# Optimization experiments

Hardware: AMD Instinct MI355X
Metric: run time of the kernel (lower is better)

The kernel has to match this reference:

```python
import jax, jax.numpy as jnp
import numpy as np

B, D_IN, HID, DEPTH = 16384, 128, 16, 8
N_INNER = 2 ** DEPTH - 1   # 255
N_LEAF = 2 ** DEPTH        # 256


def setup_inputs() -> dict:
    key = jax.random.key(0)
    ks = jax.random.split(key, 4)
    x = jax.random.normal(ks[0], (B, D_IN), jnp.float32)
    # Batched per-inner-node tiny MLP parameters (PyTorch stores one Sequential per node;
    # we stack them along a leading node axis so the math is identical but vectorized).
    W1 = jax.random.normal(ks[1], (N_INNER, D_IN, HID), jnp.float32) / np.sqrt(D_IN).astype(np.float32)
    b1 = jnp.zeros((N_INNER, HID), jnp.float32)
    W2 = jax.random.normal(ks[2], (N_INNER, HID), jnp.float32) / np.sqrt(HID).astype(np.float32)
    b2 = jnp.zeros((N_INNER,), jnp.float32)
    leaf = jax.random.normal(ks[3], (N_LEAF, 1), jnp.float32) * 0.1
    return {"x": x, "W1": W1, "b1": b1, "W2": W2, "b2": b2, "leaf": leaf}


def reference(x, W1, b1, W2, b2, leaf):
    b = x.shape[0]
    depth = int(np.log2(leaf.shape[0]))
    # All inner-node gates in one batched GEMM: p[b, n] = sigmoid(W2_n . relu(W1_n^T x_b + b1_n) + b2_n)
    h1 = jax.nn.relu(jnp.einsum('bi,nih->bnh', x, W1) + b1[None])  # [B, N_inner, hid]
    p = jax.nn.sigmoid(jnp.einsum('bnh,nh->bn', h1, W2) + b2[None])  # [B, N_inner]

    # Level-by-level probability propagation (heap-ordered nodes):
    # children of node j are 2j+1 (left, mass*(1-p)) and 2j+2 (right, mass*p).
    r = jnp.ones((b, 1), x.dtype)
    levels = []
    for l in range(depth):
        levels.append(r)
        pl = p[:, 2 ** l - 1: 2 ** (l + 1) - 1]  # probs of nodes at level l, [B, 2^l]
        # interleave (left, right) so child ordering matches heap indexing
        r = jnp.stack([r * (1.0 - pl), r * pl], axis=-1).reshape(b, 2 ** (l + 1))
    node_reach = jnp.concatenate(levels, axis=1)  # [B, N_inner]
    path_probs = r                                 # [B, N_leaf]

    h = (path_probs @ leaf)[:, 0]                  # [B]
    return (h, path_probs, p, node_reach)
```

## Files before the change

### kernel.cpp

```cpp
#include <hip/hip_runtime.h>

#define BATCH 16384
#define DIN   128
#define HIDN  16
#define NNODE 255
#define NLEAF 256
#define TR    16

typedef _Float16 half8 __attribute__((ext_vector_type(8)));
typedef _Float16 half4 __attribute__((ext_vector_type(4)));
typedef float   float4v __attribute__((ext_vector_type(4)));

__global__ __launch_bounds__(256) void k_pack(const float* __restrict__ x, const float* __restrict__ w1,
                                              const float* __restrict__ w2,
                                              half8* __restrict__ xp, half8* __restrict__ w1p,
                                              _Float16* __restrict__ w2h) {
    __shared__ float w[DIN * 17];
    int t = threadIdx.x;
    if (blockIdx.x < 1024) {
        int gid  = blockIdx.x * 256 + t;
        int lane = gid & 63;
        int kc   = (gid >> 6) & 3;
        int bt   = gid >> 8;
        const float4* src = (const float4*)(x + (size_t)(bt * 16 + (lane & 15)) * DIN + kc * 32 + ((lane >> 4) * 8));
        float4 v0 = src[0], v1 = src[1];
        half8 v;
        v[0] = (_Float16)v0.x; v[1] = (_Float16)v0.y; v[2] = (_Float16)v0.z; v[3] = (_Float16)v0.w;
        v[4] = (_Float16)v1.x; v[5] = (_Float16)v1.y; v[6] = (_Float16)v1.z; v[7] = (_Float16)v1.w;
        xp[gid] = v;
    } else {
        int n = blockIdx.x - 1024;
        const float4* src = (const float4*)(w1 + (size_t)n * (DIN * HIDN)) + t * 2;
        float4 a0 = src[0], a1 = src[1];
        int base = t * 8;
#pragma unroll
        for (int e = 0; e < 4; ++e) {
            int idx0 = base + e, idx1 = base + 4 + e;
            w[(idx0 >> 4) * 17 + (idx0 & 15)] = (&a0.x)[e];
            w[(idx1 >> 4) * 17 + (idx1 & 15)] = (&a1.x)[e];
        }
        __syncthreads();
        int L  = t & 63;
        int kc = t >> 6;
        int m  = L & 15;
        int k0 = kc * 32 + (L >> 4) * 8;
        half8 v;
#pragma unroll
        for (int j = 0; j < 8; ++j) v[j] = (_Float16)w[(k0 + j) * 17 + m];
        w1p[(size_t)n * 256 + t] = v;
        if (t < HIDN) w2h[n * HIDN + t] = (_Float16)w2[n * HIDN + t];
    }
}

__global__ __launch_bounds__(256, 3) void k_mlp(const half8* __restrict__ xp, const half8* __restrict__ w1p,
                                                const float* __restrict__ b1, const _Float16* __restrict__ w2h,
                                                const float* __restrict__ b2, float* __restrict__ p_ws) {
    int wv   = threadIdx.x >> 6;
    int lane = threadIdx.x & 63;
    int q    = lane >> 4;
    int bt0  = blockIdx.x * 16 + wv * 4;
    int n0   = blockIdx.y * 15;

    half8 bq[4][4];
#pragma unroll
    for (int t = 0; t < 4; ++t)
#pragma unroll
        for (int kc = 0; kc < 4; ++kc)
            bq[t][kc] = xp[(size_t)((bt0 + t) * 4 + kc) * 64 + lane];
    asm volatile("" ::: "memory");

    half8 a[4];
#pragma unroll
    for (int kc = 0; kc < 4; ++kc) a[kc] = w1p[(size_t)(n0 * 4 + kc) * 64 + lane];
    float4 b1f = ((const float4*)(b1 + n0 * HIDN))[q];
    half4  a2  = *(const half4*)(w2h + n0 * HIDN + q * 4);
    float  b2v = b2[n0];

    for (int i = 0; i < 15; ++i) {
        int n  = n0 + i;
        int nn = n + (i < 14 ? 1 : 0);
        half8 an[4];
#pragma unroll
        for (int kc = 0; kc < 4; ++kc) an[kc] = w1p[(size_t)(nn * 4 + kc) * 64 + lane];
        float4 b1n = ((const float4*)(b1 + nn * HIDN))[q];
        half4  a2n = *(const half4*)(w2h + nn * HIDN + q * 4);
        float  b2n = b2[nn];

#pragma unroll
        for (int t = 0; t < 4; ++t) {
            float4v acc = {b1f.x, b1f.y, b1f.z, b1f.w};
#pragma unroll
            for (int kc = 0; kc < 4; ++kc)
                acc = __builtin_amdgcn_mfma_f32_16x16x32_f16(a[kc], bq[t][kc], acc, 0, 0, 0);
            half4 rb;
#pragma unroll
            for (int r = 0; r < 4; ++r) rb[r] = (_Float16)fmaxf(acc[r], 0.f);
            float4v acc2 = {b2v, b2v, b2v, b2v};
            acc2 = __builtin_amdgcn_mfma_f32_16x16x16f16(a2, rb, acc2, 0, 0, 0);
            if (lane < 16) {
                float sg = __builtin_amdgcn_rcpf(1.f + __builtin_amdgcn_exp2f(-1.44269504088896f * acc2[0]));
                p_ws[(size_t)n * BATCH + (bt0 + t) * 16 + lane] = sg;
            }
        }
#pragma unroll
        for (int kc = 0; kc < 4; ++kc) a[kc] = an[kc];
        b1f = b1n; a2 = a2n; b2v = b2n;
    }
}

__global__ __launch_bounds__(256) void k_tree(const float* __restrict__ p_ws, const float* __restrict__ leaf,
                                              float* __restrict__ h_out, float* __restrict__ pp_out,
                                              float* __restrict__ p_out, float* __restrict__ nr_out) {
    __shared__ float sp[TR][NNODE + 2];
    int wv   = threadIdx.x >> 6;
    int lane = threadIdx.x & 63;
    int b0   = blockIdx.x * TR;
    int t    = threadIdx.x;

#pragma unroll
    for (int i = 0; i < 4; ++i) {
        int idx = i * 256 + t;
        if (idx < NNODE * 4) {
            int n = idx >> 2, b4 = (idx & 3) * 4;
            const float4 v = *(const float4*)(p_ws + (size_t)n * BATCH + b0 + b4);
            sp[b4 + 0][n] = v.x; sp[b4 + 1][n] = v.y; sp[b4 + 2][n] = v.z; sp[b4 + 3][n] = v.w;
        }
    }
    __syncthreads();

    for (int r = 0; r < TR; ++r)
        if (t < NNODE)
            __builtin_nontemporal_store(sp[r][t], &p_out[(size_t)(b0 + r) * NNODE + t]);

    for (int rr = 0; rr < 4; ++rr) {
        int i = wv * 4 + rr;
        int b = b0 + i;
        const float* P = &sp[i][0];
        float* nr = nr_out + (size_t)b * NNODE;

        float pref = 1.f;
#pragma unroll
        for (int l = 0; l < 6; ++l) {
            if ((lane & ((1 << (6 - l)) - 1)) == 0)
                __builtin_nontemporal_store(pref, &nr[(1 << l) - 1 + (lane >> (6 - l))]);
            float pv  = P[(1 << l) - 1 + (lane >> (6 - l))];
            int  bit  = (lane >> (5 - l)) & 1;
            pref *= bit ? pv : (1.f - pv);
        }
        __builtin_nontemporal_store(pref, &nr[63 + lane]);
        float p6 = P[63 + lane];
        float pl = pref * (1.f - p6);
        float pr = pref * p6;
        __builtin_nontemporal_store(pl, &nr[127 + 2 * lane]);
        __builtin_nontemporal_store(pr, &nr[128 + 2 * lane]);
        float p7a = P[127 + 2 * lane];
        float p7b = P[128 + 2 * lane];
        float4 pp;
        pp.x = pl * (1.f - p7a);
        pp.y = pl * p7a;
        pp.z = pr * (1.f - p7b);
        pp.w = pr * p7b;
        float4v ppv = {pp.x, pp.y, pp.z, pp.w};
        __builtin_nontemporal_store(ppv, (float4v*)(pp_out + (size_t)b * NLEAF + 4 * lane));
        const float4 lf = *(const float4*)(leaf + 4 * lane);
        float hs = pp.x * lf.x + pp.y * lf.y + pp.z * lf.z + pp.w * lf.w;
#pragma unroll
        for (int off = 1; off < 64; off <<= 1) hs += __shfl_xor(hs, off, 64);
        if (lane == 0) h_out[b] = hs;
    }
}

extern "C" void kernel_launch(void* const* d_in, const int* in_sizes, int n_in,
                              void* d_out, int out_size, void* d_ws, size_t ws_size,
                              hipStream_t stream) {
    const float* x    = (const float*)d_in[0];
    const float* W1   = (const float*)d_in[1];
    const float* b1   = (const float*)d_in[2];
    const float* W2   = (const float*)d_in[3];
    const float* b2   = (const float*)d_in[4];
    const float* leaf = (const float*)d_in[5];

    float* out    = (float*)d_out;
    float* h_out  = out;
    float* pp_out = out + BATCH;
    float* p_out  = pp_out + (size_t)BATCH * NLEAF;
    float* nr_out = p_out + (size_t)BATCH * NNODE;

    half8*    xp   = (half8*)d_ws;
    half8*    w1p  = xp + (size_t)1024 * 4 * 64;
    _Float16* w2h  = (_Float16*)(w1p + (size_t)NNODE * 256);
    float*    p_ws = (float*)((char*)w2h + ((NNODE * HIDN * 2 + 255) & ~255));

    hipLaunchKernelGGL(k_pack, dim3(1024 + NNODE), dim3(256), 0, stream, x, W1, W2, xp, w1p, w2h);
    hipLaunchKernelGGL(k_mlp,  dim3(64, 17), dim3(256), 0, stream, xp, w1p, b1, w2h, b2, p_ws);
    hipLaunchKernelGGL(k_tree, dim3(BATCH / TR), dim3(256), 0, stream,
                       p_ws, leaf, h_out, pp_out, p_out, nr_out);
}
```

Baseline: 130.2 us.

## Fuse MLP gate computation and tree propagation into one kernel via LDS

Merges the MLP gate kernel and the tree-propagation kernel. Each block now handles 64 batch rows, with each of its four waves computing every fourth node, and the sigmoid outputs go into a shared-memory tile instead of a global workspace. The tree pass then reads that tile directly. This removes the global write and read of the 16 MB probability workspace and one launch. The cost is only 256 blocks of 256 threads at one block per CU, so each wave runs a long serial loop over about 64 nodes and the GPU has less parallelism to hide latency.

```diff
diff --git a/kernel.cpp b/kernel.cpp
--- a/kernel.cpp
+++ b/kernel.cpp
@@ -5,7 +5,6 @@
 #define HIDN  16
 #define NNODE 255
 #define NLEAF 256
-#define TR    16
 
 typedef _Float16 half8 __attribute__((ext_vector_type(8)));
 typedef _Float16 half4 __attribute__((ext_vector_type(4)));
@@ -52,14 +51,16 @@
     }
 }
 
-__global__ __launch_bounds__(256, 3) void k_mlp(const half8* __restrict__ xp, const half8* __restrict__ w1p,
-                                                const float* __restrict__ b1, const _Float16* __restrict__ w2h,
-                                                const float* __restrict__ b2, float* __restrict__ p_ws) {
+__global__ __launch_bounds__(256, 1) void k_fused(const half8* __restrict__ xp, const half8* __restrict__ w1p,
+                                                  const float* __restrict__ b1, const _Float16* __restrict__ w2h,
+                                                  const float* __restrict__ b2, const float* __restrict__ leaf,
+                                                  float* __restrict__ h_out, float* __restrict__ pp_out,
+                                                  float* __restrict__ p_out, float* __restrict__ nr_out) {
+    __shared__ float sp[64][260];
     int wv   = threadIdx.x >> 6;
     int lane = threadIdx.x & 63;
     int q    = lane >> 4;
-    int bt0  = blockIdx.x * 16 + wv * 4;
-    int n0   = blockIdx.y * 15;
+    int bt0  = blockIdx.x * 4;
 
     half8 bq[4][4];
 #pragma unroll
@@ -69,16 +70,17 @@
             bq[t][kc] = xp[(size_t)((bt0 + t) * 4 + kc) * 64 + lane];
     asm volatile("" ::: "memory");
 
+    int cnt = (wv < 3) ? 64 : 63;
+    int n   = wv;
     half8 a[4];
 #pragma unroll
-    for (int kc = 0; kc < 4; ++kc) a[kc] = w1p[(size_t)(n0 * 4 + kc) * 64 + lane];
-    float4 b1f = ((const float4*)(b1 + n0 * HIDN))[q];
-    half4  a2  = *(const half4*)(w2h + n0 * HIDN + q * 4);
-    float  b2v = b2[n0];
+    for (int kc = 0; kc < 4; ++kc) a[kc] = w1p[(size_t)(n * 4 + kc) * 64 + lane];
+    float4 b1f = ((const float4*)(b1 + n * HIDN))[q];
+    half4  a2  = *(const half4*)(w2h + n * HIDN + q * 4);
+    float  b2v = b2[n];
 
-    for (int i = 0; i < 15; ++i) {
-        int n  = n0 + i;
-        int nn = n + (i < 14 ? 1 : 0);
+    for (int i = 0; i < cnt; ++i) {
+        int nn = n + ((i + 1 < cnt) ? 4 : 0);
         half8 an[4];
 #pragma unroll
         for (int kc = 0; kc < 4; ++kc) an[kc] = w1p[(size_t)(nn * 4 + kc) * 64 + lane];
@@ -97,46 +99,30 @@
             for (int r = 0; r < 4; ++r) rb[r] = (_Float16)fmaxf(acc[r], 0.f);
             float4v acc2 = {b2v, b2v, b2v, b2v};
             acc2 = __builtin_amdgcn_mfma_f32_16x16x16f16(a2, rb, acc2, 0, 0, 0);
-            if (lane < 16) {
-                float sg = __builtin_amdgcn_rcpf(1.f + __builtin_amdgcn_exp2f(-1.44269504088896f * acc2[0]));
-                p_ws[(size_t)n * BATCH + (bt0 + t) * 16 + lane] = sg;
-            }
+            if (lane < 16)
+                sp[t * 16 + lane][n] =
+                    __builtin_amdgcn_rcpf(1.f + __builtin_amdgcn_exp2f(-1.44269504088896f * acc2[0]));
         }
 #pragma unroll
         for (int kc = 0; kc < 4; ++kc) a[kc] = an[kc];
         b1f = b1n; a2 = a2n; b2v = b2n;
-    }
-}
-
-__global__ __launch_bounds__(256) void k_tree(const float* __restrict__ p_ws, const float* __restrict__ leaf,
-                                              float* __restrict__ h_out, float* __restrict__ pp_out,
-                                              float* __restrict__ p_out, float* __restrict__ nr_out) {
-    __shared__ float sp[TR][NNODE + 2];
-    int wv   = threadIdx.x >> 6;
-    int lane = threadIdx.x & 63;
-    int b0   = blockIdx.x * TR;
-    int t    = threadIdx.x;
-
-#pragma unroll
-    for (int i = 0; i < 4; ++i) {
-        int idx = i * 256 + t;
-        if (idx < NNODE * 4) {
-            int n = idx >> 2, b4 = (idx & 3) * 4;
-            const float4 v = *(const float4*)(p_ws + (size_t)n * BATCH + b0 + b4);
-            sp[b4 + 0][n] = v.x; sp[b4 + 1][n] = v.y; sp[b4 + 2][n] = v.z; sp[b4 + 3][n] = v.w;
-        }
+        n = nn;
     }
     __syncthreads();
 
-    for (int r = 0; r < TR; ++r)
-        if (t < NNODE)
-            __builtin_nontemporal_store(sp[r][t], &p_out[(size_t)(b0 + r) * NNODE + t]);
+    const float4 lf = *(const float4*)(leaf + 4 * lane);
+    for (int rr = 0; rr < 16; ++rr) {
+        int r = wv * 16 + rr;
+        int b = blockIdx.x * 64 + r;
+        const float* P = &sp[r][0];
+        float* nr = nr_out + (size_t)b * NNODE;
 
-    for (int rr = 0; rr < 4; ++rr) {
-        int i = wv * 4 + rr;
-        int b = b0 + i;
-        const float* P = &sp[i][0];
-        float* nr = nr_out + (size_t)b * NNODE;
+#pragma unroll
+        for (int c = 0; c < 4; ++c) {
+            int idx = c * 64 + lane;
+            if (idx < NNODE)
+                __builtin_nontemporal_store(P[idx], &p_out[(size_t)b * NNODE + idx]);
+        }
 
         float pref = 1.f;
 #pragma unroll
@@ -155,15 +141,13 @@
         __builtin_nontemporal_store(pr, &nr[128 + 2 * lane]);
         float p7a = P[127 + 2 * lane];
         float p7b = P[128 + 2 * lane];
-        float4 pp;
-        pp.x = pl * (1.f - p7a);
-        pp.y = pl * p7a;
-        pp.z = pr * (1.f - p7b);
-        pp.w = pr * p7b;
-        float4v ppv = {pp.x, pp.y, pp.z, pp.w};
-        __builtin_nontemporal_store(ppv, (float4v*)(pp_out + (size_t)b * NLEAF + 4 * lane));
-        const float4 lf = *(const float4*)(leaf + 4 * lane);
-        float hs = pp.x * lf.x + pp.y * lf.y + pp.z * lf.z + pp.w * lf.w;
+        float4v pp;
+        pp[0] = pl * (1.f - p7a);
+        pp[1] = pl * p7a;
+        pp[2] = pr * (1.f - p7b);
+        pp[3] = pr * p7b;
+        __builtin_nontemporal_store(pp, (float4v*)(pp_out + (size_t)b * NLEAF + 4 * lane));
+        float hs = pp[0] * lf.x + pp[1] * lf.y + pp[2] * lf.z + pp[3] * lf.w;
 #pragma unroll
         for (int off = 1; off < 64; off <<= 1) hs += __shfl_xor(hs, off, 64);
         if (lane == 0) h_out[b] = hs;
@@ -189,10 +173,8 @@
     half8*    xp   = (half8*)d_ws;
     half8*    w1p  = xp + (size_t)1024 * 4 * 64;
     _Float16* w2h  = (_Float16*)(w1p + (size_t)NNODE * 256);
-    float*    p_ws = (float*)((char*)w2h + ((NNODE * HIDN * 2 + 255) & ~255));
 
-    hipLaunchKernelGGL(k_pack, dim3(1024 + NNODE), dim3(256), 0, stream, x, W1, W2, xp, w1p, w2h);
-    hipLaunchKernelGGL(k_mlp,  dim3(64, 17), dim3(256), 0, stream, xp, w1p, b1, w2h, b2, p_ws);
-    hipLaunchKernelGGL(k_tree, dim3(BATCH / TR), dim3(256), 0, stream,
-                       p_ws, leaf, h_out, pp_out, p_out, nr_out);
+    hipLaunchKernelGGL(k_pack,  dim3(1024 + NNODE), dim3(256), 0, stream, x, W1, W2, xp, w1p, w2h);
+    hipLaunchKernelGGL(k_fused, dim3(256),          dim3(256), 0, stream,
+                       xp, w1p, b1, w2h, b2, leaf, h_out, pp_out, p_out, nr_out);
 }
```

Measured after the change: 139.8 us. 1.07x slower.
